# Optimization experiments

Measured on AMD Instinct MI355X. Metric: run time of the kernel, lower is better.

The kernel has to match this reference:

```python
import jax, jax.numpy as jnp
import numpy as np

N, D, H = 4096, 512, 8
HD = D // H
KEEP_RATIO = 0.5
EPS = 1e-6

def setup_inputs() -> dict:
    key = jax.random.key(0)
    ks = jax.random.split(key, 10)
    s = 1.0 / np.sqrt(D)
    return {
        'stock_feats': jax.random.normal(ks[0], (N, D), jnp.float32),
        'z_primary': jax.random.normal(ks[1], (1, D), jnp.float32),
        'z_secondary': jax.random.normal(ks[2], (1, D), jnp.float32),
        'Wq': jax.random.normal(ks[3], (D, D), jnp.float32) * s,
        'Wk': jax.random.normal(ks[4], (D, D), jnp.float32) * s,
        'Wv': jax.random.normal(ks[5], (D, D), jnp.float32) * s,
        'Wg': jax.random.normal(ks[6], (D, 2 * D), jnp.float32) * s,
        'bg': jnp.zeros((D,), jnp.float32),
        'Wag': jax.random.normal(ks[7], (D, 2 * D), jnp.float32) * s,
        'bag': jnp.zeros((D,), jnp.float32),
        'norm_w': jnp.ones((D,), jnp.float32),
        'Wo': jax.random.normal(ks[8], (D, D), jnp.float32) * s,
        'bo': jnp.zeros((D,), jnp.float32),
    }

def reference(stock_feats, z_primary, z_secondary, Wq, Wk, Wv, Wg, bg, Wag, bag, norm_w, Wo, bo):
    scale = 1.0 / np.sqrt(HD)
    nodes = jnp.concatenate([z_primary, z_secondary, stock_feats], axis=0)  # [N+2, D]
    # regime-gated queries
    z_concat = jnp.concatenate([z_primary, z_secondary], axis=-1)  # [1, 2D]
    regime_mod = jax.nn.sigmoid(z_concat @ Wg.T + bg)              # [1, D]
    q = ((stock_feats @ Wq.T) * regime_mod).reshape(N, H, HD)
    k = (nodes @ Wk.T).reshape(N + 2, H, HD)
    v = (nodes @ Wv.T).reshape(N + 2, H, HD)
    scores = jnp.einsum('nhd,mhd->nhm', q, k) * scale              # [N, H, N+2]
    raw_scores = scores.mean(axis=1)                               # [N, N+2]
    # top-k mask over stock (non-anchor) columns
    anchor_scores = scores[..., :2]
    stock_scores = scores[..., 2:]                                 # [N, H, N]
    k_keep = max(5, int(N * KEEP_RATIO))
    topk_val = jax.lax.top_k(stock_scores, k_keep)[0]
    threshold = topk_val[..., -1:]
    stock_scores = jnp.where(stock_scores >= threshold, stock_scores, -1e9)
    scores_m = jnp.concatenate([anchor_scores, stock_scores], axis=-1)
    attn = jax.nn.softmax(scores_m, axis=-1)                       # [N, H, N+2]
    out = jnp.einsum('nhm,mhd->nhd', attn, v).reshape(N, D)
    out = out @ Wo.T + bo
    # alpha guard: gated residual + RMSNorm
    gate = jax.nn.sigmoid(jnp.concatenate([stock_feats, out], axis=-1) @ Wag.T + bag)
    gr = stock_feats + gate * out
    rms = jax.lax.rsqrt(jnp.mean(gr * gr, axis=-1, keepdims=True) + EPS)
    final_out = gr * rms * norm_w
    return (final_out, raw_scores, gate.mean(), attn.mean(axis=1))
```

## Files before the change

kernel.cpp:

```cpp
#include <hip/hip_runtime.h>
#include <hip/hip_fp16.h>
#include <math.h>

#define NS 4096
#define DIM 512
#define NH 8
#define HD 64
#define M2 4098
#define MPAD 4224
#define KKEEP 2048u

#define OUT_F 0
#define OUT_R 2097152
#define OUT_G 18882560
#define OUT_A 18882561

typedef __attribute__((ext_vector_type(8))) short bf16x8;
typedef __attribute__((ext_vector_type(4))) float f32x4;

__device__ __forceinline__ float sigmoidf_(float x) { return 1.0f / (1.0f + __expf(-x)); }

__device__ __forceinline__ unsigned short btrunc(float f) {
  unsigned u = __float_as_uint(f);
  u = u + 0x7FFFu + ((u >> 16) & 1u);
  return (unsigned short)(u >> 16);
}
__device__ __forceinline__ float bton(unsigned short h) {
  return __uint_as_float(((unsigned)h) << 16);
}

__device__ __forceinline__ void scan_pick(unsigned c0, unsigned c1, unsigned c2, unsigned c3,
                                          unsigned k_rem, int lane,
                                          unsigned& bsel_out, unsigned& nxt_out) {
  unsigned run = c0 + c1 + c2 + c3;
  #pragma unroll
  for (int off = 1; off < 64; off <<= 1) {
    unsigned o_ = __shfl_down(run, off, 64);
    if (lane + off < 64) run += o_;
  }
  unsigned s0 = run, s1 = run - c0, s2 = s1 - c1, s3 = s2 - c2, s4 = s3 - c3;
  int which = -1;
  if      (s0 >= k_rem && s1 < k_rem) which = 0;
  else if (s1 >= k_rem && s2 < k_rem) which = 1;
  else if (s2 >= k_rem && s3 < k_rem) which = 2;
  else if (s3 >= k_rem && s4 < k_rem) which = 3;
  unsigned long long bal = __ballot(which >= 0);
  int src = (int)__ffsll(bal) - 1;
  unsigned nxtv = (which == 0) ? s1 : (which == 1) ? s2 : (which == 2) ? s3 : s4;
  unsigned bsel = (unsigned)(4 * lane + (which < 0 ? 0 : which));
  bsel_out = (unsigned)__shfl((int)bsel, src, 64);
  nxt_out  = (unsigned)__shfl((int)nxtv, src, 64);
}

__global__ __launch_bounds__(256) void regime_kernel(
    const float* __restrict__ zp, const float* __restrict__ zs,
    const float* __restrict__ Wg, const float* __restrict__ bg,
    float* __restrict__ regime) {
  __shared__ float zc[1024];
  int t = threadIdx.x;
  for (int i = t; i < 512; i += 256) { zc[i] = zp[i]; zc[512 + i] = zs[i]; }
  __syncthreads();
  for (int j = t; j < 512; j += 256) {
    const float4* w = (const float4*)(Wg + (size_t)j * 1024);
    float acc = 0.f;
    #pragma unroll 8
    for (int i = 0; i < 256; i++) {
      float4 wv = w[i];
      acc += wv.x * zc[4*i] + wv.y * zc[4*i+1] + wv.z * zc[4*i+2] + wv.w * zc[4*i+3];
    }
    regime[j] = sigmoidf_(acc + bg[j]);
  }
}

__global__ __launch_bounds__(256) void conv_bf(
    const float* __restrict__ src, unsigned short* __restrict__ dst, int n4) {
  int i4 = blockIdx.x * 256 + threadIdx.x;
  if (i4 >= n4) return;
  float4 v = *(const float4*)(src + (size_t)i4 * 4);
  ushort4 o; o.x = btrunc(v.x); o.y = btrunc(v.y); o.z = btrunc(v.z); o.w = btrunc(v.w);
  *(ushort4*)(dst + (size_t)i4 * 4) = o;
}

__global__ __launch_bounds__(256) void build_nodes_bf(
    const float* __restrict__ zp, const float* __restrict__ zs,
    const float* __restrict__ sf, unsigned short* __restrict__ nb) {
  int i4 = blockIdx.x * 256 + threadIdx.x;
  if (i4 >= (M2 * DIM) / 4) return;
  int idx = i4 * 4;
  int m = idx >> 9, c = idx & 511;
  const float* src = (m == 0) ? (zp + c) : (m == 1) ? (zs + c)
                               : (sf + (size_t)(m - 2) * 512 + c);
  float4 v = *(const float4*)src;
  ushort4 o; o.x = btrunc(v.x); o.y = btrunc(v.y); o.z = btrunc(v.z); o.w = btrunc(v.w);
  *(ushort4*)(nb + idx) = o;
}

#define LSTR 40
__global__ __launch_bounds__(256) void gemm_bf16(
    const unsigned short* __restrict__ A, const unsigned short* __restrict__ B,
    const float* __restrict__ bias, const float* __restrict__ cscale,
    const float* __restrict__ rscale,
    float* __restrict__ Cf, unsigned short* __restrict__ Cb,
    int M, int N, int K, int lda, int ldb, int ldc, float scale, int mode,
    size_t sA, size_t sB, size_t sC, size_t sR) {
  __shared__ unsigned short As[128 * LSTR];
  __shared__ unsigned short Bs[128 * LSTR];
  const int z = blockIdx.z;
  A += (size_t)z * sA;
  B += (size_t)z * sB;
  if (Cf) Cf += (size_t)z * sC;
  if (Cb) Cb += (size_t)z * sC;
  if (rscale) rscale += (size_t)z * sR;
  const int t = threadIdx.x;
  const int w = t >> 6, lane = t & 63;
  const int wr = w >> 1, wc = w & 1;
  const int lr = lane & 15, lg = lane >> 4;
  const int bm = blockIdx.y * 128, bn = blockIdx.x * 128;
  f32x4 acc[4][4] = {};
  for (int k0 = 0; k0 < K; k0 += 32) {
    #pragma unroll
    for (int i = 0; i < 2; i++) {
      int q = t + i * 256;
      int row = q >> 2;
      int ko = (q & 3) * 8;
      bf16x8 av = {};
      int gr = bm + row;
      if (gr < M) av = *(const bf16x8*)(A + (size_t)gr * lda + k0 + ko);
      *(bf16x8*)(As + row * LSTR + ko) = av;
      bf16x8 bv = {};
      int gbr = bn + row;
      if (gbr < N) bv = *(const bf16x8*)(B + (size_t)gbr * ldb + k0 + ko);
      *(bf16x8*)(Bs + row * LSTR + ko) = bv;
    }
    __syncthreads();
    {
      bf16x8 af[4], bfr[4];
      #pragma unroll
      for (int i = 0; i < 4; i++)
        af[i] = *(const bf16x8*)(As + (64 * wr + 16 * i + lr) * LSTR + lg * 8);
      #pragma unroll
      for (int j = 0; j < 4; j++)
        bfr[j] = *(const bf16x8*)(Bs + (64 * wc + 16 * j + lr) * LSTR + lg * 8);
      #pragma unroll
      for (int i = 0; i < 4; i++)
        #pragma unroll
        for (int j = 0; j < 4; j++)
          acc[i][j] = __builtin_amdgcn_mfma_f32_16x16x32_bf16(af[i], bfr[j], acc[i][j], 0, 0, 0);
    }
    __syncthreads();
  }
  #pragma unroll
  for (int i = 0; i < 4; i++) {
    #pragma unroll
    for (int j = 0; j < 4; j++) {
      #pragma unroll
      for (int q = 0; q < 4; q++) {
        int row = bm + 64 * wr + 16 * i + lg * 4 + q;
        int col = bn + 64 * wc + 16 * j + lr;
        if (row < M && col < N) {
          float v = acc[i][j][q] * scale;
          if (bias)   v += bias[col];
          if (cscale) v *= cscale[col];
          if (rscale) v *= rscale[row];
          if (mode == 0)      Cf[(size_t)row * ldc + col] = v;
          else if (mode == 1) Cb[(size_t)row * ldc + col] = btrunc(v);
          else                Cb[(size_t)col * ldc + row] = btrunc(v);
        }
      }
    }
  }
}

__global__ __launch_bounds__(256) void select_softmax(
    unsigned short* __restrict__ S, float* __restrict__ Zg) {
  __shared__ unsigned short keys[4][MPAD];
  __shared__ unsigned hist[4][256];
  const int w = threadIdx.x >> 6, lane = threadIdx.x & 63;
  const size_t row = (size_t)blockIdx.x * 4 + w;
  unsigned short* kr = keys[w];
  unsigned* hw = hist[w];
  unsigned short* g = S + row * MPAD;
  unsigned a0k = 0, a1k = 0;

  hw[lane] = 0u; hw[lane + 64] = 0u; hw[lane + 128] = 0u; hw[lane + 192] = 0u;
  unsigned maxkey = 0;
  #pragma unroll
  for (int c = 0; c < 9; ++c) {
    if (c < 8 || lane < 16) {
      uint4 v = *(const uint4*)(g + c * 512 + lane * 8);
      unsigned* pv = (unsigned*)&v;
      int mb = c * 512 + lane * 8;
      #pragma unroll
      for (int p2 = 0; p2 < 4; ++p2) {
        unsigned pk = pv[p2], outw = 0;
        #pragma unroll
        for (int e = 0; e < 2; ++e) {
          int m = mb + 2 * p2 + e;
          unsigned u = (e == 0) ? (pk & 0xFFFFu) : (pk >> 16);
          unsigned key = u ^ ((u & 0x8000u) ? 0xFFFFu : 0x8000u);
          if (m < 2) { if (m == 0) a0k = key; else a1k = key; key = 0u; }
          else if (m >= M2) key = 0u;
          outw |= key << (16 * e);
          atomicAdd(&hw[key >> 8], 1u);
          if (key > maxkey) maxkey = key;
        }
        *(unsigned*)(kr + mb + 2 * p2) = outw;
      }
    }
  }
  if (a0k > maxkey) maxkey = a0k;
  if (a1k > maxkey) maxkey = a1k;
  #pragma unroll
  for (int off = 32; off > 0; off >>= 1) {
    unsigned o_ = (unsigned)__shfl_xor((int)maxkey, off, 64);
    if (o_ > maxkey) maxkey = o_;
  }
  float lmax = bton((unsigned short)(maxkey ^ ((maxkey & 0x8000u) ? 0x8000u : 0xFFFFu)));

  unsigned tb, k_rem = KKEEP;
  {
    unsigned c0 = hw[4*lane], c1 = hw[4*lane+1], c2 = hw[4*lane+2], c3 = hw[4*lane+3];
    unsigned nxtv;
    scan_pick(c0, c1, c2, c3, k_rem, lane, tb, nxtv);
    k_rem -= nxtv;
  }

  hw[lane] = 0u; hw[lane + 64] = 0u; hw[lane + 128] = 0u; hw[lane + 192] = 0u;
  #pragma unroll
  for (int c = 0; c < 9; ++c) {
    if (c < 8 || lane < 16) {
      uint4 v = *(const uint4*)(kr + c * 512 + lane * 8);
      const unsigned* pv = (const unsigned*)&v;
      #pragma unroll
      for (int p2 = 0; p2 < 4; ++p2) {
        unsigned lo = pv[p2] & 0xFFFFu, hi = pv[p2] >> 16;
        if ((lo >> 8) == tb) atomicAdd(&hw[lo & 255u], 1u);
        if ((hi >> 8) == tb) atomicAdd(&hw[hi & 255u], 1u);
      }
    }
  }
  unsigned thrkey;
  {
    unsigned c0 = hw[4*lane], c1 = hw[4*lane+1], c2 = hw[4*lane+2], c3 = hw[4*lane+3];
    unsigned bsel, nxtv;
    scan_pick(c0, c1, c2, c3, k_rem, lane, bsel, nxtv);
    thrkey = (tb << 8) | bsel;
  }

  float lsum = 0.f;
  #pragma unroll
  for (int c = 0; c < 9; ++c) {
    if (c < 8 || lane < 16) {
      uint4 v = *(const uint4*)(kr + c * 512 + lane * 8);
      unsigned* pv = (unsigned*)&v;
      #pragma unroll
      for (int p2 = 0; p2 < 4; ++p2) {
        unsigned pk = pv[p2], outw = 0;
        bool anc = (c == 0 && lane == 0 && p2 == 0);
        if (anc) pk = a0k | (a1k << 16);
        #pragma unroll
        for (int e = 0; e < 2; ++e) {
          unsigned key = (e == 0) ? (pk & 0xFFFFu) : (pk >> 16);
          bool kept = anc || (key >= thrkey);
          unsigned short us = (unsigned short)(key ^ ((key & 0x8000u) ? 0x8000u : 0xFFFFu));
          float ev = kept ? __expf(bton(us) - lmax) : 0.f;
          unsigned short eb = btrunc(ev);
          lsum += bton(eb);
          outw |= ((unsigned)eb) << (16 * e);
        }
        pv[p2] = outw;
      }
      *(uint4*)(g + c * 512 + lane * 8) = v;
    }
  }
  #pragma unroll
  for (int off = 32; off > 0; off >>= 1) lsum += __shfl_xor(lsum, off, 64);
  if (lane == 0) Zg[row] = 1.0f / lsum;
}

__global__ __launch_bounds__(256) void am_reduce(
    const unsigned short* __restrict__ P, const float* __restrict__ Zg,
    float* __restrict__ outA) {
  int tid = blockIdx.x * 256 + threadIdx.x;
  int n = tid / 513, cm = tid % 513;
  int bm = cm * 8;
  float s[8] = {};
  #pragma unroll
  for (int h = 0; h < 8; ++h) {
    float zi = Zg[h * 4096 + n];
    uint4 v = *(const uint4*)(P + ((size_t)h * 4096 + n) * MPAD + bm);
    const unsigned* pv = (const unsigned*)&v;
    #pragma unroll
    for (int p2 = 0; p2 < 4; ++p2) {
      s[2*p2]   += bton((unsigned short)(pv[p2] & 0xFFFFu)) * zi;
      s[2*p2+1] += bton((unsigned short)(pv[p2] >> 16)) * zi;
    }
  }
  float* dst = outA + (size_t)n * M2 + bm;
  #pragma unroll
  for (int k = 0; k < 8; ++k)
    if (bm + k < M2) dst[k] = s[k] * 0.125f;
}

#define SROWB 8464
#define QOFF  (16 * SROWB)
#define HOFF  (QOFF + 16 * 72 * 2)
#define AOFF  (HOFF + 16 * 256 * 4)
#define SMEMSZ (AOFF + 64)

__global__ __launch_bounds__(1024) void fused_attn(
    const unsigned short* __restrict__ Qbf, const unsigned short* __restrict__ Kbf,
    const unsigned short* __restrict__ Vt, unsigned short* __restrict__ aobf,
    float* __restrict__ attn_mean_out) {
  extern __shared__ char dsm[];
  unsigned short* qt = (unsigned short*)(dsm + QOFF);
  unsigned* hist = (unsigned*)(dsm + HOFF);
  unsigned short* anchk = (unsigned short*)(dsm + AOFF);
  const int n0 = blockIdx.x * 16;
  const int t = threadIdx.x;
  const int w = t >> 6, lane = t & 63;
  const int lr = lane & 15, lg = lane >> 4;
  unsigned* hw = hist + w * 256;
  const int r = w;
  const unsigned swz = (unsigned)((r & 7) << 4);

  for (int h = 0; h < NH; ++h) {
    qt[(t >> 6) * 72 + (t & 63)] = Qbf[(size_t)(n0 + (t >> 6)) * DIM + h * HD + (t & 63)];
    __syncthreads();
    {
      bf16x8 a0 = *(const bf16x8*)(qt + lr * 72 + lg * 8);
      bf16x8 a1 = *(const bf16x8*)(qt + lr * 72 + 32 + lg * 8);
      #pragma unroll
      for (int f = 0; f < 17; ++f) {
        if (f < 16 || w < 8) {
          int m0 = (w + 16 * f) * 16;
          const unsigned short* kp = Kbf + (size_t)(m0 + lr) * DIM + h * HD + lg * 8;
          bf16x8 b0 = *(const bf16x8*)(kp);
          bf16x8 b1 = *(const bf16x8*)(kp + 32);
          f32x4 c = {0.f, 0.f, 0.f, 0.f};
          c = __builtin_amdgcn_mfma_f32_16x16x32_bf16(a0, b0, c, 0, 0, 0);
          c = __builtin_amdgcn_mfma_f32_16x16x32_bf16(a1, b1, c, 0, 0, 0);
          int m = m0 + lr;
          #pragma unroll
          for (int q = 0; q < 4; ++q) {
            int rr = lg * 4 + q;
            unsigned short us = btrunc(c[q] * 0.125f);
            unsigned key = (unsigned)us ^ ((us & 0x8000u) ? 0xFFFFu : 0x8000u);
            unsigned short stor = (m >= M2 || m < 2) ? (unsigned short)0 : (unsigned short)key;
            *(unsigned short*)(dsm + rr * SROWB + ((2 * m) ^ ((rr & 7) << 4))) = stor;
            if (m < 2) anchk[rr * 2 + m] = (unsigned short)key;
          }
        }
      }
    }
    __syncthreads();

    float invZ;
    {
      unsigned maxkey = 0;
      hw[lane] = 0u; hw[lane + 64] = 0u; hw[lane + 128] = 0u; hw[lane + 192] = 0u;
      #pragma unroll
      for (int c = 0; c < 9; ++c) {
        if (c < 8 || lane < 16) {
          uint4 pk4 = *(const uint4*)(dsm + r * SROWB + (((unsigned)(c * 1024 + lane * 16)) ^ swz));
          const unsigned* pw = (const unsigned*)&pk4;
          #pragma unroll
          for (int p2 = 0; p2 < 4; ++p2) {
            unsigned pk = pw[p2];
            unsigned lo = pk & 0xFFFFu, hi = pk >> 16;
            atomicAdd(&hw[lo >> 8], 1u);
            atomicAdd(&hw[hi >> 8], 1u);
            if (lo > maxkey) maxkey = lo;
            if (hi > maxkey) maxkey = hi;
          }
        }
      }
      #pragma unroll
      for (int off = 32; off > 0; off >>= 1) {
        unsigned o_ = (unsigned)__shfl_xor((int)maxkey, off, 64);
        if (o_ > maxkey) maxkey = o_;
      }
      {
        unsigned a0 = anchk[2 * r], a1 = anchk[2 * r + 1];
        if (a0 > maxkey) maxkey = a0;
        if (a1 > maxkey) maxkey = a1;
      }
      float lmax = bton((unsigned short)(maxkey ^ ((maxkey & 0x8000u) ? 0x8000u : 0xFFFFu)));

      unsigned tb, k_rem = KKEEP;
      {
        unsigned c0 = hw[4*lane], c1 = hw[4*lane+1], c2 = hw[4*lane+2], c3 = hw[4*lane+3];
        unsigned nxtv;
        scan_pick(c0, c1, c2, c3, k_rem, lane, tb, nxtv);
        k_rem -= nxtv;
      }
      hw[lane] = 0u; hw[lane + 64] = 0u; hw[lane + 128] = 0u; hw[lane + 192] = 0u;
      #pragma unroll
      for (int c = 0; c < 9; ++c) {
        if (c < 8 || lane < 16) {
          uint4 pk4 = *(const uint4*)(dsm + r * SROWB + (((unsigned)(c * 1024 + lane * 16)) ^ swz));
          const unsigned* pw = (const unsigned*)&pk4;
          #pragma unroll
          for (int p2 = 0; p2 < 4; ++p2) {
            unsigned pk = pw[p2];
            unsigned lo = pk & 0xFFFFu, hi = pk >> 16;
            if ((lo >> 8) == tb) atomicAdd(&hw[lo & 255u], 1u);
            if ((hi >> 8) == tb) atomicAdd(&hw[hi & 255u], 1u);
          }
        }
      }
      unsigned thrkey;
      {
        unsigned c0 = hw[4*lane], c1 = hw[4*lane+1], c2 = hw[4*lane+2], c3 = hw[4*lane+3];
        unsigned bsel, nxtv;
        scan_pick(c0, c1, c2, c3, k_rem, lane, bsel, nxtv);
        thrkey = (tb << 8) | bsel;
      }

      float lsum = 0.f;
      #pragma unroll
      for (int c = 0; c < 9; ++c) {
        if (c < 8 || lane < 16) {
          char* ap = dsm + r * SROWB + (((unsigned)(c * 1024 + lane * 16)) ^ swz);
          uint4 pk4 = *(const uint4*)ap;
          unsigned* pw = (unsigned*)&pk4;
          #pragma unroll
          for (int p2 = 0; p2 < 4; ++p2) {
            unsigned pk = pw[p2];
            bool anc = (c == 0 && lane == 0 && p2 == 0);
            if (anc) pk = (unsigned)anchk[2 * r] | ((unsigned)anchk[2 * r + 1] << 16);
            unsigned outw = 0;
            #pragma unroll
            for (int e = 0; e < 2; ++e) {
              unsigned key = (e == 0) ? (pk & 0xFFFFu) : (pk >> 16);
              bool kept = anc || (key >= thrkey);
              unsigned short us = (unsigned short)(key ^ ((key & 0x8000u) ? 0x8000u : 0xFFFFu));
              float evf = kept ? __expf(bton(us) - lmax) : 0.f;
              unsigned short eb = btrunc(evf);
              lsum += bton(eb);
              outw |= ((unsigned)eb) << (16 * e);
            }
            pw[p2] = outw;
          }
          *(uint4*)ap = pk4;
        }
      }
      #pragma unroll
      for (int off = 32; off > 0; off >>= 1) lsum += __shfl_xor(lsum, off, 64);
      invZ = 1.0f / lsum;
      for (int c = 0; c < 9; ++c) {
        if (c < 8 || lane < 16) {
          const char* ap = dsm + r * SROWB + (((unsigned)(c * 1024 + lane * 16)) ^ swz);
          uint4 e4 = *(const uint4*)ap;
          const unsigned* pw = (const unsigned*)&e4;
          int bm = c * 512 + lane * 8;
          float* base = attn_mean_out + (size_t)(n0 + r) * M2 + bm;
          #pragma unroll
          for (int p2 = 0; p2 < 4; ++p2) {
            float v0 = bton((unsigned short)(pw[p2] & 0xFFFFu)) * invZ * 0.125f;
            float v1 = bton((unsigned short)(pw[p2] >> 16)) * invZ * 0.125f;
            int m = bm + 2 * p2;
            if (m < M2)     { if (h == 0) base[2*p2] = v0;   else base[2*p2] += v0; }
            if (m + 1 < M2) { if (h == 0) base[2*p2+1] = v1; else base[2*p2+1] += v1; }
          }
        }
      }
    }
    __syncthreads();

    {
      f32x4 o0 = {0.f,0.f,0.f,0.f}, o1 = o0, o2 = o0, o3 = o0;
      const unsigned short* Vb = Vt + (size_t)(h * HD) * MPAD;
      #pragma unroll
      for (int ks = 0; ks < 9; ++ks) {
        if (ks < 8 || w < 4) {
          int kk = (w + 16 * ks) * 32 + lg * 8;
          bf16x8 a = *(const bf16x8*)(dsm + lr * SROWB + ((2 * kk) ^ ((lr & 7) << 4)));
          {
            bf16x8 b0 = *(const bf16x8*)(Vb + (size_t)(lr) * MPAD + kk);
            bf16x8 b1 = *(const bf16x8*)(Vb + (size_t)(16 + lr) * MPAD + kk);
            o0 = __builtin_amdgcn_mfma_f32_16x16x32_bf16(a, b0, o0, 0, 0, 0);
            o1 = __builtin_amdgcn_mfma_f32_16x16x32_bf16(a, b1, o1, 0, 0, 0);
          }
          {
            bf16x8 b2 = *(const bf16x8*)(Vb + (size_t)(32 + lr) * MPAD + kk);
            bf16x8 b3 = *(const bf16x8*)(Vb + (size_t)(48 + lr) * MPAD + kk);
            o2 = __builtin_amdgcn_mfma_f32_16x16x32_bf16(a, b2, o2, 0, 0, 0);
            o3 = __builtin_amdgcn_mfma_f32_16x16x32_bf16(a, b3, o3, 0, 0, 0);
          }
        }
      }
      __syncthreads();
      float* part = (float*)dsm;
      #pragma unroll
      for (int q = 0; q < 4; q++) {
        int row = lg * 4 + q;
        part[w * 1024 + row * 64 +      lr] = o0[q];
        part[w * 1024 + row * 64 + 16 + lr] = o1[q];
        part[w * 1024 + row * 64 + 32 + lr] = o2[q];
        part[w * 1024 + row * 64 + 48 + lr] = o3[q];
      }
      __syncthreads();
      {
        float s = 0.f;
        #pragma unroll
        for (int ww = 0; ww < 16; ++ww) s += part[ww * 1024 + t];
        aobf[(size_t)(n0 + (t >> 6)) * DIM + h * HD + (t & 63)] = btrunc(s * invZ);
      }
    }
  }
}

__global__ __launch_bounds__(256) void cat_bf(
    const unsigned short* __restrict__ sfbf, const float* __restrict__ pj,
    unsigned short* __restrict__ cat) {
  int i4 = blockIdx.x * 256 + threadIdx.x;
  if (i4 >= (4096 * 1024) / 4) return;
  int idx = i4 * 4;
  int n = idx >> 10, c = idx & 1023;
  if (c < 512) {
    *(ushort4*)(cat + idx) = *(const ushort4*)(sfbf + (size_t)n * 512 + c);
  } else {
    float4 v = *(const float4*)(pj + (size_t)n * 512 + (c - 512));
    ushort4 o; o.x = btrunc(v.x); o.y = btrunc(v.y); o.z = btrunc(v.z); o.w = btrunc(v.w);
    *(ushort4*)(cat + idx) = o;
  }
}

__global__ __launch_bounds__(256) void final_kernel(
    const float* __restrict__ sf, const float* __restrict__ pj,
    const float* __restrict__ gl, const float* __restrict__ norm_w,
    float* __restrict__ outf, float* __restrict__ gpart) {
  int n = blockIdx.x, t = threadIdx.x;
  __shared__ float red[256];
  size_t base = (size_t)n * 512;
  float g0 = sigmoidf_(gl[base + t]);
  float g1 = sigmoidf_(gl[base + 256 + t]);
  float x0 = sf[base + t], x1 = sf[base + 256 + t];
  float p0 = pj[base + t], p1 = pj[base + 256 + t];
  float gr0 = x0 + g0 * p0, gr1 = x1 + g1 * p1;

  red[t] = g0 + g1;
  __syncthreads();
  for (int off = 128; off > 0; off >>= 1) {
    if (t < off) red[t] += red[t + off];
    __syncthreads();
  }
  if (t == 0) gpart[n] = red[0];
  __syncthreads();

  red[t] = gr0 * gr0 + gr1 * gr1;
  __syncthreads();
  for (int off = 128; off > 0; off >>= 1) {
    if (t < off) red[t] += red[t + off];
    __syncthreads();
  }
  float rms = rsqrtf(red[0] * (1.0f / 512.0f) + 1e-6f);
  outf[base + t] = gr0 * rms * norm_w[t];
  outf[base + 256 + t] = gr1 * rms * norm_w[256 + t];
}

__global__ __launch_bounds__(256) void gate_reduce(
    const float* __restrict__ gpart, float* __restrict__ out_scalar) {
  __shared__ float red[256];
  int t = threadIdx.x;
  float s = 0.f;
  for (int i = t; i < 4096; i += 256) s += gpart[i];
  red[t] = s;
  __syncthreads();
  for (int off = 128; off > 0; off >>= 1) {
    if (t < off) red[t] += red[t + off];
    __syncthreads();
  }
  if (t == 0) out_scalar[0] = red[0] * (1.0f / (4096.0f * 512.0f));
}

extern "C" void kernel_launch(void* const* d_in, const int* in_sizes, int n_in,
                              void* d_out, int out_size, void* d_ws, size_t ws_size,
                              hipStream_t stream) {
  const float* sf  = (const float*)d_in[0];
  const float* zp  = (const float*)d_in[1];
  const float* zs  = (const float*)d_in[2];
  const float* Wq  = (const float*)d_in[3];
  const float* Wk  = (const float*)d_in[4];
  const float* Wv  = (const float*)d_in[5];
  const float* Wg  = (const float*)d_in[6];
  const float* bg  = (const float*)d_in[7];
  const float* Wag = (const float*)d_in[8];
  const float* bag = (const float*)d_in[9];
  const float* nw  = (const float*)d_in[10];
  const float* Wo  = (const float*)d_in[11];
  const float* bo  = (const float*)d_in[12];

  float* out  = (float*)d_out;
  float* outF = out + OUT_F;
  float* outR = out + OUT_R;
  float* outG = out + OUT_G;
  float* outA = out + OUT_A;

  char* W = (char*)d_ws;
  float*          regime  = (float*)(W + 0);
  float*          gpart   = (float*)(W + 2048);
  unsigned short* sfbf    = (unsigned short*)(W + 18432);
  unsigned short* nodesbf = (unsigned short*)(W + 4212736);
  unsigned short* Qbf     = (unsigned short*)(W + 8409088);
  unsigned short* Kbf     = (unsigned short*)(W + 12603392);
  unsigned short* Vt      = (unsigned short*)(W + 16928768);
  unsigned short* aobf    = (unsigned short*)(W + 21254144);
  unsigned short* catbf   = (unsigned short*)(W + 25448448);
  unsigned short* Wqbf    = (unsigned short*)(W + 33837056);
  unsigned short* Wkbf    = (unsigned short*)(W + 34361344);
  unsigned short* Wvbf    = (unsigned short*)(W + 34885632);
  unsigned short* Wobf    = (unsigned short*)(W + 35409920);
  unsigned short* Wagbf   = (unsigned short*)(W + 35934208);
  float*          pj      = (float*)(W + 36982784);
  float*          gl      = (float*)(W + 4212736);
  unsigned short* Splane  = (unsigned short*)(W + 45371392);
  float*          Zg      = (float*)(W + 322195456);
  const size_t need_s = 322195456ull + 131072ull;
  const int use_s = (ws_size >= need_s) ? 1 : 0;

  hipFuncSetAttribute((const void*)fused_attn,
                      hipFuncAttributeMaxDynamicSharedMemorySize, SMEMSZ);

  regime_kernel<<<1, 256, 0, stream>>>(zp, zs, Wg, bg, regime);
  conv_bf<<<2048, 256, 0, stream>>>(sf, sfbf, 524288);
  build_nodes_bf<<<2049, 256, 0, stream>>>(zp, zs, sf, nodesbf);
  conv_bf<<<256, 256, 0, stream>>>(Wq, Wqbf, 65536);
  conv_bf<<<256, 256, 0, stream>>>(Wk, Wkbf, 65536);
  conv_bf<<<256, 256, 0, stream>>>(Wv, Wvbf, 65536);
  conv_bf<<<256, 256, 0, stream>>>(Wo, Wobf, 65536);
  conv_bf<<<512, 256, 0, stream>>>(Wag, Wagbf, 131072);
  hipMemsetAsync(Kbf, 0, 4325376, stream);
  hipMemsetAsync(Vt, 0, 4325376, stream);

  gemm_bf16<<<dim3(4, 32, 1), 256, 0, stream>>>(sfbf, Wqbf, nullptr, regime, nullptr, nullptr, Qbf,
                                                4096, 512, 512, 512, 512, 512, 1.0f, 1, 0, 0, 0, 0);
  gemm_bf16<<<dim3(4, 33, 1), 256, 0, stream>>>(nodesbf, Wkbf, nullptr, nullptr, nullptr, nullptr, Kbf,
                                                M2, 512, 512, 512, 512, 512, 1.0f, 1, 0, 0, 0, 0);
  gemm_bf16<<<dim3(4, 33, 1), 256, 0, stream>>>(nodesbf, Wvbf, nullptr, nullptr, nullptr, nullptr, Vt,
                                                M2, 512, 512, 512, 512, MPAD, 1.0f, 2, 0, 0, 0, 0);

  gemm_bf16<<<dim3(33, 32, 1), 256, 0, stream>>>(Qbf, Kbf, nullptr, nullptr, nullptr, outR, nullptr,
                                                 4096, M2, 512, 512, 512, M2, 0.015625f, 0, 0, 0, 0, 0);

  if (use_s) {
    gemm_bf16<<<dim3(33, 32, 8), 256, 0, stream>>>(Qbf, Kbf, nullptr, nullptr, nullptr, nullptr, Splane,
                                                   4096, M2, 64, 512, 512, MPAD, 0.125f, 1,
                                                   64, 64, (size_t)4096 * MPAD, 0);
    select_softmax<<<8192, 256, 0, stream>>>(Splane, Zg);
    gemm_bf16<<<dim3(1, 32, 8), 256, 0, stream>>>(Splane, Vt, nullptr, nullptr, Zg, nullptr, aobf,
                                                  4096, 64, MPAD, MPAD, MPAD, 512, 1.0f, 1,
                                                  (size_t)4096 * MPAD, (size_t)64 * MPAD, 64, 4096);
    am_reduce<<<8208, 256, 0, stream>>>(Splane, Zg, outA);
  } else {
    fused_attn<<<256, 1024, SMEMSZ, stream>>>(Qbf, Kbf, Vt, aobf, outA);
  }

  gemm_bf16<<<dim3(4, 32, 1), 256, 0, stream>>>(aobf, Wobf, bo, nullptr, nullptr, pj, nullptr,
                                                4096, 512, 512, 512, 512, 512, 1.0f, 0, 0, 0, 0, 0);
  cat_bf<<<4096, 256, 0, stream>>>(sfbf, pj, catbf);
  gemm_bf16<<<dim3(4, 32, 1), 256, 0, stream>>>(catbf, Wagbf, bag, nullptr, nullptr, gl, nullptr,
                                                4096, 512, 1024, 1024, 1024, 512, 1.0f, 0, 0, 0, 0, 0);
  final_kernel<<<4096, 256, 0, stream>>>(sf, pj, gl, nw, outF, gpart);
  gate_reduce<<<1, 256, 0, stream>>>(gpart, outG);
}
```

Measured before the change: 922.0 us.

## Fuse head-mean attention reduction into softmax and split-K the PV GEMM

Each select_softmax block now handles all 8 heads of one query row with 512 threads. The normalized probabilities stay in shared memory so the head-mean attn output is written directly, and the separate am_reduce pass that re-read the whole probability plane is removed. The P·V GEMM is split along K into two chunks that accumulate with float atomics into a zeroed fp32 buffer, which is then converted to bf16. This adds a memset, atomics and a conversion kernel, and it needs a larger workspace, so the fallback fused path runs if the workspace is too small.

```diff
diff --git a/kernel.cpp b/kernel.cpp
--- a/kernel.cpp
+++ b/kernel.cpp
@@ -102,15 +102,16 @@
     const float* __restrict__ rscale,
     float* __restrict__ Cf, unsigned short* __restrict__ Cb,
     int M, int N, int K, int lda, int ldb, int ldc, float scale, int mode,
-    size_t sA, size_t sB, size_t sC, size_t sR) {
+    size_t sA, size_t sB, size_t sC, size_t sR, int kz, int ksz) {
   __shared__ unsigned short As[128 * LSTR];
   __shared__ unsigned short Bs[128 * LSTR];
   const int z = blockIdx.z;
-  A += (size_t)z * sA;
-  B += (size_t)z * sB;
-  if (Cf) Cf += (size_t)z * sC;
-  if (Cb) Cb += (size_t)z * sC;
-  if (rscale) rscale += (size_t)z * sR;
+  const int zh = z / kz, zc = z - zh * kz;
+  A += (size_t)zh * sA + (size_t)zc * ksz;
+  B += (size_t)zh * sB + (size_t)zc * ksz;
+  if (Cf) Cf += (size_t)zh * sC;
+  if (Cb) Cb += (size_t)zh * sC;
+  if (rscale) rscale += (size_t)zh * sR;
   const int t = threadIdx.x;
   const int w = t >> 6, lane = t & 63;
   const int wr = w >> 1, wc = w & 1;
@@ -164,21 +165,26 @@
           if (rscale) v *= rscale[row];
           if (mode == 0)      Cf[(size_t)row * ldc + col] = v;
           else if (mode == 1) Cb[(size_t)row * ldc + col] = btrunc(v);
-          else                Cb[(size_t)col * ldc + row] = btrunc(v);
-        }
-      }
-    }
-  }
-}
-
-__global__ __launch_bounds__(256) void select_softmax(
-    unsigned short* __restrict__ S, float* __restrict__ Zg) {
-  __shared__ unsigned short keys[4][MPAD];
-  __shared__ unsigned hist[4][256];
+          else if (mode == 2) Cb[(size_t)col * ldc + row] = btrunc(v);
+          else                atomicAdd(&Cf[(size_t)row * ldc + col], v);
+        }
+      }
+    }
+  }
+}
+
+#define SSMEM (8 * MPAD * 2 + 8 * 256 * 4 + 32)
+__global__ __launch_bounds__(512) void select_softmax(
+    unsigned short* __restrict__ S, float* __restrict__ Zg, float* __restrict__ outA) {
+  extern __shared__ char sm[];
+  unsigned short* keys = (unsigned short*)sm;
+  unsigned* hist = (unsigned*)(sm + 8 * MPAD * 2);
+  float* Zs = (float*)(sm + 8 * MPAD * 2 + 8 * 256 * 4);
   const int w = threadIdx.x >> 6, lane = threadIdx.x & 63;
-  const size_t row = (size_t)blockIdx.x * 4 + w;
-  unsigned short* kr = keys[w];
-  unsigned* hw = hist[w];
+  const int n = blockIdx.x;
+  const size_t row = (size_t)w * 4096 + n;
+  unsigned short* kr = keys + w * MPAD;
+  unsigned* hw = hist + w * 256;
   unsigned short* g = S + row * MPAD;
   unsigned a0k = 0, a1k = 0;
 
@@ -270,36 +276,23 @@
         }
         pv[p2] = outw;
       }
+      *(uint4*)(kr + c * 512 + lane * 8) = v;
       *(uint4*)(g + c * 512 + lane * 8) = v;
     }
   }
   #pragma unroll
   for (int off = 32; off > 0; off >>= 1) lsum += __shfl_xor(lsum, off, 64);
-  if (lane == 0) Zg[row] = 1.0f / lsum;
-}
-
-__global__ __launch_bounds__(256) void am_reduce(
-    const unsigned short* __restrict__ P, const float* __restrict__ Zg,
-    float* __restrict__ outA) {
-  int tid = blockIdx.x * 256 + threadIdx.x;
-  int n = tid / 513, cm = tid % 513;
-  int bm = cm * 8;
-  float s[8] = {};
-  #pragma unroll
-  for (int h = 0; h < 8; ++h) {
-    float zi = Zg[h * 4096 + n];
-    uint4 v = *(const uint4*)(P + ((size_t)h * 4096 + n) * MPAD + bm);
-    const unsigned* pv = (const unsigned*)&v;
+  float invZ = 1.0f / lsum;
+  if (lane == 0) { Zg[row] = invZ; Zs[w] = invZ; }
+  __syncthreads();
+
+  for (int m = threadIdx.x; m < M2; m += 512) {
+    float s = 0.f;
     #pragma unroll
-    for (int p2 = 0; p2 < 4; ++p2) {
-      s[2*p2]   += bton((unsigned short)(pv[p2] & 0xFFFFu)) * zi;
-      s[2*p2+1] += bton((unsigned short)(pv[p2] >> 16)) * zi;
-    }
-  }
-  float* dst = outA + (size_t)n * M2 + bm;
-  #pragma unroll
-  for (int k = 0; k < 8; ++k)
-    if (bm + k < M2) dst[k] = s[k] * 0.125f;
+    for (int h = 0; h < 8; ++h)
+      s += bton(keys[h * MPAD + m]) * Zs[h];
+    outA[(size_t)n * M2 + m] = s * 0.125f;
+  }
 }
 
 #define SROWB 8464
@@ -617,11 +610,14 @@
   float*          gl      = (float*)(W + 4212736);
   unsigned short* Splane  = (unsigned short*)(W + 45371392);
   float*          Zg      = (float*)(W + 322195456);
-  const size_t need_s = 322195456ull + 131072ull;
+  float*          aopf    = (float*)(W + 322326528);
+  const size_t need_s = 330715136ull;
   const int use_s = (ws_size >= need_s) ? 1 : 0;
 
   hipFuncSetAttribute((const void*)fused_attn,
                       hipFuncAttributeMaxDynamicSharedMemorySize, SMEMSZ);
+  hipFuncSetAttribute((const void*)select_softmax,
+                      hipFuncAttributeMaxDynamicSharedMemorySize, SSMEM);
 
   regime_kernel<<<1, 256, 0, stream>>>(zp, zs, Wg, bg, regime);
   conv_bf<<<2048, 256, 0, stream>>>(sf, sfbf, 524288);
@@ -635,33 +631,34 @@
   hipMemsetAsync(Vt, 0, 4325376, stream);
 
   gemm_bf16<<<dim3(4, 32, 1), 256, 0, stream>>>(sfbf, Wqbf, nullptr, regime, nullptr, nullptr, Qbf,
-                                                4096, 512, 512, 512, 512, 512, 1.0f, 1, 0, 0, 0, 0);
+                                                4096, 512, 512, 512, 512, 512, 1.0f, 1, 0, 0, 0, 0, 1, 0);
   gemm_bf16<<<dim3(4, 33, 1), 256, 0, stream>>>(nodesbf, Wkbf, nullptr, nullptr, nullptr, nullptr, Kbf,
-                                                M2, 512, 512, 512, 512, 512, 1.0f, 1, 0, 0, 0, 0);
+                                                M2, 512, 512, 512, 512, 512, 1.0f, 1, 0, 0, 0, 0, 1, 0);
   gemm_bf16<<<dim3(4, 33, 1), 256, 0, stream>>>(nodesbf, Wvbf, nullptr, nullptr, nullptr, nullptr, Vt,
-                                                M2, 512, 512, 512, 512, MPAD, 1.0f, 2, 0, 0, 0, 0);
+                                                M2, 512, 512, 512, 512, MPAD, 1.0f, 2, 0, 0, 0, 0, 1, 0);
 
   gemm_bf16<<<dim3(33, 32, 1), 256, 0, stream>>>(Qbf, Kbf, nullptr, nullptr, nullptr, outR, nullptr,
-                                                 4096, M2, 512, 512, 512, M2, 0.015625f, 0, 0, 0, 0, 0);
+                                                 4096, M2, 512, 512, 512, M2, 0.015625f, 0, 0, 0, 0, 0, 1, 0);
 
   if (use_s) {
     gemm_bf16<<<dim3(33, 32, 8), 256, 0, stream>>>(Qbf, Kbf, nullptr, nullptr, nullptr, nullptr, Splane,
                                                    4096, M2, 64, 512, 512, MPAD, 0.125f, 1,
-                                                   64, 64, (size_t)4096 * MPAD, 0);
-    select_softmax<<<8192, 256, 0, stream>>>(Splane, Zg);
-    gemm_bf16<<<dim3(1, 32, 8), 256, 0, stream>>>(Splane, Vt, nullptr, nullptr, Zg, nullptr, aobf,
-                                                  4096, 64, MPAD, MPAD, MPAD, 512, 1.0f, 1,
-                                                  (size_t)4096 * MPAD, (size_t)64 * MPAD, 64, 4096);
-    am_reduce<<<8208, 256, 0, stream>>>(Splane, Zg, outA);
+                                                   64, 64, (size_t)4096 * MPAD, 0, 1, 0);
+    select_softmax<<<4096, 512, SSMEM, stream>>>(Splane, Zg, outA);
+    hipMemsetAsync(aopf, 0, 8388608, stream);
+    gemm_bf16<<<dim3(1, 32, 16), 256, 0, stream>>>(Splane, Vt, nullptr, nullptr, Zg, aopf, nullptr,
+                                                   4096, 64, 2112, MPAD, MPAD, 512, 1.0f, 3,
+                                                   (size_t)4096 * MPAD, (size_t)64 * MPAD, 64, 4096, 2, 2112);
+    conv_bf<<<2048, 256, 0, stream>>>(aopf, aobf, 524288);
   } else {
     fused_attn<<<256, 1024, SMEMSZ, stream>>>(Qbf, Kbf, Vt, aobf, outA);
   }
 
   gemm_bf16<<<dim3(4, 32, 1), 256, 0, stream>>>(aobf, Wobf, bo, nullptr, nullptr, pj, nullptr,
-                                                4096, 512, 512, 512, 512, 512, 1.0f, 0, 0, 0, 0, 0);
+                                                4096, 512, 512, 512, 512, 512, 1.0f, 0, 0, 0, 0, 0, 1, 0);
   cat_bf<<<4096, 256, 0, stream>>>(sfbf, pj, catbf);
   gemm_bf16<<<dim3(4, 32, 1), 256, 0, stream>>>(catbf, Wagbf, bag, nullptr, nullptr, gl, nullptr,
-                                                4096, 512, 1024, 1024, 1024, 512, 1.0f, 0, 0, 0, 0, 0);
+                                                4096, 512, 1024, 1024, 1024, 512, 1.0f, 0, 0, 0, 0, 0, 1, 0);
   final_kernel<<<4096, 256, 0, stream>>>(sf, pj, gl, nw, outF, gpart);
   gate_reduce<<<1, 256, 0, stream>>>(gpart, outG);
 }
```

Measured after the change: 889.1 us. -3.6%, faster.
